# Kernel tuning notes

Measured on AMD Instinct MI355X. Metric: run time of the kernel, lower is better.

## Reference

```python
import jax, jax.numpy as jnp
import numpy as np

PAD = 1
THRESH = 10.0


def setup_inputs() -> dict:
    key = jax.random.key(0)
    k1, k2, k3 = jax.random.split(key, 3)
    x = jax.random.normal(k1, (8, 16, 62, 62), dtype=jnp.float32)
    W = jax.random.normal(k2, (32, 16, 3, 3), dtype=jnp.float32)
    b = jax.random.normal(k3, (32,), dtype=jnp.float32)
    return {"x": x, "W": W, "b": b}


def reference(x, W, b):
    # ZeroPad2d(padding) on all four sides
    x = jnp.pad(x, ((0, 0), (0, 0), (PAD, PAD), (PAD, PAD)))
    T, C, xr, xc = x.shape
    O, _, wr, wc = W.shape
    L = xr * xc

    # get_xfft_thresh: 1D FFT over flattened HxW, zero coeffs with |Re| < thresh
    xf = jnp.fft.fft(x.reshape(T, C, L))                      # (T,C,L) complex
    xf = jnp.where(jnp.abs(xf.real) < THRESH, jnp.zeros_like(xf), xf)

    # get_Wfft: zero-pad kernel to (xr,xc) bottom/right, flatten, reverse along
    # length (flipud(flip([0,1])) nets to a flip of the last axis only), then FFT
    Wp = jnp.pad(W, ((0, 0), (0, 0), (0, xr - wr), (0, xc - wc))).reshape(O, C, L)
    Wf = jnp.fft.fft(Wp[:, :, ::-1])                          # (O,C,L) complex

    # fftConv1D, batched over (image, out_channel):
    y = jnp.fft.ifft(xf[:, None, :, :] * Wf[None, :, :, :]).real  # (T,O,C,L)
    # torch.roll(y, 1) with no dims rolls the FLATTENED (C*L) tensor by 1
    y = jnp.roll(y.reshape(T, O, C * L), 1, axis=-1).reshape(T, O, C, xr, xc)
    y = y.sum(axis=2)                                         # sum over in-channels
    ans_r, ans_c = xr - wr + 1, xc - wc + 1
    y = y[:, :, :ans_r, :ans_c]
    return y + b[None, :, None, None]
```

## Files before the change

kernel.cpp:

```cpp
#include <hip/hip_runtime.h>
#include <math.h>

#define TWO_PI 6.28318530717958647692f
#define NT     1024
#define RPW    4
#define PITCH  65
#define THRESH 10.0f
#define C64    0.995184726672196886f
#define S64    0.098017140329560602f
#define C4096  0.999998823451701879f
#define S4096  0.001533980186284766f

typedef float v2f __attribute__((ext_vector_type(2)));

__device__ __forceinline__ int brev6(int x) {
    return (int)(__brev((unsigned)x) >> 26);
}

__device__ __forceinline__ v2f cmul_add(v2f a, v2f b, v2f acc) {
    acc += (v2f){a.x, a.x} * b;
    acc += (v2f){a.y, a.y} * (v2f){-b.y, b.x};
    return acc;
}

template<int R>
__device__ __forceinline__ void fft64_dif(float (&re)[R], float (&im)[R],
                                          int lane, float sign) {
    #pragma unroll
    for (int h = 32; h >= 1; h >>= 1) {
        int j = lane & (h - 1);
        float ang = sign * (TWO_PI / 64.0f) * (float)(j * (32 / h));
        float wr, wi;
        __sincosf(ang, &wi, &wr);
        bool upper = (lane & h) != 0;
        float cwr = upper ? wr : 1.0f;
        float cwi = upper ? wi : 0.0f;
        float sgn = upper ? -1.0f : 1.0f;
        #pragma unroll
        for (int m = 0; m < R; ++m) {
            float orr = __shfl_xor(re[m], h, 64);
            float oii = __shfl_xor(im[m], h, 64);
            float ar = fmaf(sgn, re[m], orr);
            float ai = fmaf(sgn, im[m], oii);
            re[m] = ar * cwr - ai * cwi;
            im[m] = ar * cwi + ai * cwr;
        }
    }
}

template<int R>
__device__ __forceinline__ void fft64_dit(float (&re)[R], float (&im)[R],
                                          int lane, float sign) {
    #pragma unroll
    for (int h = 1; h <= 32; h <<= 1) {
        int j = lane & (h - 1);
        float ang = sign * (TWO_PI / 64.0f) * (float)(j * (32 / h));
        float wr, wi;
        __sincosf(ang, &wi, &wr);
        bool upper = (lane & h) != 0;
        float cwr = upper ? wr : 1.0f;
        float cwi = upper ? wi : 0.0f;
        float sgn = upper ? -1.0f : 1.0f;
        #pragma unroll
        for (int m = 0; m < R; ++m) {
            float tr = re[m] * cwr - im[m] * cwi;
            float ti = re[m] * cwi + im[m] * cwr;
            float orr = __shfl_xor(tr, h, 64);
            float oii = __shfl_xor(ti, h, 64);
            re[m] = fmaf(sgn, tr, orr);
            im[m] = fmaf(sgn, ti, oii);
        }
    }
}

__global__ __launch_bounds__(NT) void fwdA_kernel(const float* __restrict__ x,
                                                  float2* __restrict__ Xa) {
    __shared__ float sre[64 * 33];
    __shared__ float sim[64 * 33];
    const int task = blockIdx.x >> 1;
    const int h    = blockIdx.x & 1;
    const int tid  = threadIdx.x;
    const int lane = tid & 63;
    const int w    = tid >> 6;
    const float* xr = x + (size_t)task * 62 * 62;
    for (int idx = tid; idx < 64 * 32; idx += NT) {
        int r = idx >> 5, j = idx & 31;
        int n2 = 32 * h + j;
        float v = 0.0f;
        if (r >= 1 && r <= 62 && n2 >= 1 && n2 <= 62)
            v = xr[(r - 1) * 62 + (n2 - 1)];
        sre[r * 33 + j] = v;
    }
    __syncthreads();
    float re[2], im[2];
    #pragma unroll
    for (int m = 0; m < 2; ++m) {
        re[m] = sre[lane * 33 + (w * 2 + m)];
        im[m] = 0.0f;
    }
    fft64_dif<2>(re, im, lane, -1.0f);
    __syncthreads();
    const int k1 = brev6(lane);
    #pragma unroll
    for (int m = 0; m < 2; ++m) {
        int j  = w * 2 + m;
        int n2 = 32 * h + j;
        float cr, ci;
        __sincosf(-(TWO_PI / 4096.0f) * (float)(k1 * n2), &ci, &cr);
        sre[k1 * 33 + j] = re[m] * cr - im[m] * ci;
        sim[k1 * 33 + j] = re[m] * ci + im[m] * cr;
    }
    __syncthreads();
    float2* Arow = Xa + (size_t)task * 4096;
    for (int idx = tid; idx < 64 * 32; idx += NT) {
        int k = idx >> 5, j = idx & 31;
        Arow[k * 64 + 32 * h + j] = make_float2(sre[k * 33 + j], sim[k * 33 + j]);
    }
}

__global__ __launch_bounds__(NT) void fwdB_kernel(const float2* __restrict__ Xa,
                                                  float2* __restrict__ X) {
    const int task = blockIdx.x >> 1;
    const int h    = blockIdx.x & 1;
    const int tid  = threadIdx.x;
    const int lane = tid & 63;
    const int w    = tid >> 6;
    const float2* Arow = Xa + (size_t)task * 4096;
    float re[2], im[2];
    #pragma unroll
    for (int m = 0; m < 2; ++m) {
        float2 xv = Arow[(32 * h + w * 2 + m) * 64 + lane];
        re[m] = xv.x; im[m] = xv.y;
    }
    fft64_dif<2>(re, im, lane, -1.0f);
    float2* Xrow = X + (size_t)task * 4096;
    #pragma unroll
    for (int m = 0; m < 2; ++m) {
        float rr = re[m], ii = im[m];
        if (fabsf(rr) < THRESH) { rr = 0.0f; ii = 0.0f; }
        Xrow[(32 * h + w * 2 + m) * 64 + lane] = make_float2(rr, ii);
    }
}

__global__ __launch_bounds__(NT, 4) void conv_kernel(const float2* __restrict__ X,
                                                     const float* __restrict__ W,
                                                     const float* __restrict__ b,
                                                     float* __restrict__ out) {
    __shared__ float sre[64 * PITCH];
    __shared__ float sim[64 * PITCH];
    const int t    = blockIdx.x >> 5;
    const int o    = blockIdx.x & 31;
    const int tid  = threadIdx.x;
    const int lane = tid & 63;
    const int w    = tid >> 6;

    const int k2 = brev6(lane);
    float elr, eli;
    __sincosf((TWO_PI / 64.0f) * (float)k2, &eli, &elr);

    v2f uv[RPW], vv[RPW], v2v[RPW];
    {
        float cur, cui, cvr, cvi;
        __sincosf((TWO_PI / 16.0f) * (float)w, &cui, &cur);
        __sincosf((TWO_PI / 1024.0f) * (float)w, &cvi, &cvr);
        #pragma unroll
        for (int m = 0; m < RPW; ++m) {
            uv[m] = (v2f){cur, cui};
            float vvr = cvr * elr - cvi * eli;
            float vvi = cvr * eli + cvi * elr;
            vv[m]  = (v2f){vvr, vvi};
            v2v[m] = (v2f){vvr * vvr - vvi * vvi, 2.0f * vvr * vvi};
            float nur = cur * C64 - cui * S64;
            cui = cur * S64 + cui * C64; cur = nur;
            float nvr = cvr * C4096 - cvi * S4096;
            cvi = cvr * S4096 + cvi * C4096; cvr = nvr;
        }
    }

    v2f S[RPW];
    #pragma unroll
    for (int m = 0; m < RPW; ++m) S[m] = (v2f){0.0f, 0.0f};

    const float2* Xt = X + (size_t)t * 16 * 4096 + (w * (RPW * 64) + lane);
    const float*  wo = W + o * 144;

    v2f xb[RPW];
    #pragma unroll
    for (int m = 0; m < RPW; ++m) {
        float2 q = Xt[m * 64];
        xb[m] = (v2f){q.x, q.y};
    }
    #pragma unroll 1
    for (int c = 0; c < 16; ++c) {
        v2f xn[RPW];
        if (c < 15) {
            const float2* xp = Xt + (c + 1) * 4096;
            #pragma unroll
            for (int m = 0; m < RPW; ++m) {
                float2 q = xp[m * 64];
                xn[m] = (v2f){q.x, q.y};
            }
        }
        const float wa0 = wo[c*9+0], wa1 = wo[c*9+1], wa2 = wo[c*9+2];
        const float wa3 = wo[c*9+3], wa4 = wo[c*9+4], wa5 = wo[c*9+5];
        const float wa6 = wo[c*9+6], wa7 = wo[c*9+7], wa8 = wo[c*9+8];
        #pragma unroll
        for (int m = 0; m < RPW; ++m) {
            v2f v = vv[m], v2 = v2v[m], u = uv[m];
            v2f h0 = (v2f){wa0, 0.0f}; h0 += v * wa1; h0 += v2 * wa2;
            v2f h1 = (v2f){wa3, 0.0f}; h1 += v * wa4; h1 += v2 * wa5;
            v2f h2 = (v2f){wa6, 0.0f}; h2 += v * wa7; h2 += v2 * wa8;
            v2f in = cmul_add(u, h2, h1);
            v2f P  = cmul_add(u, in, h0);
            S[m]   = cmul_add(xb[m], P, S[m]);
        }
        #pragma unroll
        for (int m = 0; m < RPW; ++m) xb[m] = xn[m];
    }

    float re[RPW], im[RPW];
    #pragma unroll
    for (int m = 0; m < RPW; ++m) { re[m] = S[m].x; im[m] = S[m].y; }
    fft64_dit<RPW>(re, im, lane, +1.0f);
    {
        float cr, ci, sr, si;
        __sincosf((TWO_PI / 1024.0f) * (float)(lane * w), &ci, &cr);
        __sincosf((TWO_PI / 4096.0f) * (float)lane, &si, &sr);
        #pragma unroll
        for (int m = 0; m < RPW; ++m) {
            float rr = re[m] * cr - im[m] * ci;
            im[m]    = re[m] * ci + im[m] * cr;
            re[m]    = rr;
            float nr = cr * sr - ci * si;
            ci = cr * si + ci * sr; cr = nr;
        }
    }
    #pragma unroll
    for (int m = 0; m < RPW; ++m) {
        int k1 = w * RPW + m;
        sre[k1 * PITCH + lane] = re[m];
        sim[k1 * PITCH + lane] = im[m];
    }
    __syncthreads();
    #pragma unroll
    for (int m = 0; m < RPW; ++m) {
        int n2 = w * RPW + m;
        re[m] = sre[lane * PITCH + n2];
        im[m] = sim[lane * PITCH + n2];
    }
    fft64_dif<RPW>(re, im, lane, +1.0f);
    __syncthreads();
    const int n1 = brev6(lane);
    #pragma unroll
    for (int m = 0; m < RPW; ++m) {
        int n2 = w * RPW + m;
        sre[n1 * PITCH + n2] = re[m];
    }
    __syncthreads();
    const float bias = b[o];
    float* orow = out + (size_t)blockIdx.x * 62 * 62;
    for (int idx = tid; idx < 62 * 62; idx += NT) {
        int r = idx / 62, s = idx - r * 62;
        orow[idx] = sre[r * PITCH + s] * (1.0f / 4096.0f) + bias;
    }
}

extern "C" void kernel_launch(void* const* d_in, const int* in_sizes, int n_in,
                              void* d_out, int out_size, void* d_ws, size_t ws_size,
                              hipStream_t stream) {
    const float* x = (const float*)d_in[0];
    const float* W = (const float*)d_in[1];
    const float* b = (const float*)d_in[2];
    float* out = (float*)d_out;
    float2* Xa = (float2*)d_ws;
    float2* X  = Xa + 128 * 4096;

    fwdA_kernel<<<dim3(256), dim3(NT), 0, stream>>>(x, Xa);
    fwdB_kernel<<<dim3(256), dim3(NT), 0, stream>>>(Xa, X);
    conv_kernel<<<dim3(256), dim3(NT), 0, stream>>>(X, W, b, out);
}
```

Before: 86.39 us.

## Exploit Hermitian symmetry to compute only half the spectrum in forward FFT and conv

The forward FFT stage now stores and processes only rows 0..32 of the 64x64 spectrum, since the input is real. The conv kernel accumulates the frequency product for only those 33 rows and rebuilds the conjugate-symmetric half from shared memory before the inverse FFT. This roughly halves the per-channel complex multiply-accumulate work and the X traffic. In exchange it adds an extra shared-memory round trip with two barriers, plus divergent work for the lone middle row handled by wave 0. The symmetry only holds if the threshold mask preserves conjugate pairs, which it does because it tests only |Re|.

After: 82.87 us. 4.1% less time.

```diff
diff --git a/kernel.cpp b/kernel.cpp
--- a/kernel.cpp
+++ b/kernel.cpp
@@ -6,10 +6,8 @@
 #define RPW    4
 #define PITCH  65
 #define THRESH 10.0f
-#define C64    0.995184726672196886f
-#define S64    0.098017140329560602f
-#define C4096  0.999998823451701879f
-#define S4096  0.001533980186284766f
+#define C128   0.998795456205172393f
+#define S128   0.049067674327418015f
 
 typedef float v2f __attribute__((ext_vector_type(2)));
 
@@ -114,7 +112,9 @@
     float2* Arow = Xa + (size_t)task * 4096;
     for (int idx = tid; idx < 64 * 32; idx += NT) {
         int k = idx >> 5, j = idx & 31;
-        Arow[k * 64 + 32 * h + j] = make_float2(sre[k * 33 + j], sim[k * 33 + j]);
+        if (k <= 32)
+            Arow[k * 64 + 32 * h + j] =
+                make_float2(sre[k * 33 + j], sim[k * 33 + j]);
     }
 }
 
@@ -125,20 +125,25 @@
     const int tid  = threadIdx.x;
     const int lane = tid & 63;
     const int w    = tid >> 6;
+    if (h == 1 && w > 0) return;
     const float2* Arow = Xa + (size_t)task * 4096;
     float re[2], im[2];
     #pragma unroll
     for (int m = 0; m < 2; ++m) {
-        float2 xv = Arow[(32 * h + w * 2 + m) * 64 + lane];
+        int row = 32 * h + w * 2 + m;
+        float2 xv = (row <= 32) ? Arow[row * 64 + lane] : make_float2(0.f, 0.f);
         re[m] = xv.x; im[m] = xv.y;
     }
     fft64_dif<2>(re, im, lane, -1.0f);
     float2* Xrow = X + (size_t)task * 4096;
     #pragma unroll
     for (int m = 0; m < 2; ++m) {
-        float rr = re[m], ii = im[m];
-        if (fabsf(rr) < THRESH) { rr = 0.0f; ii = 0.0f; }
-        Xrow[(32 * h + w * 2 + m) * 64 + lane] = make_float2(rr, ii);
+        int row = 32 * h + w * 2 + m;
+        if (row <= 32) {
+            float rr = re[m], ii = im[m];
+            if (fabsf(rr) < THRESH) { rr = 0.0f; ii = 0.0f; }
+            Xrow[row * 64 + lane] = make_float2(rr, ii);
+        }
     }
 }
 
@@ -158,69 +163,86 @@
     float elr, eli;
     __sincosf((TWO_PI / 64.0f) * (float)k2, &eli, &elr);
 
-    v2f uv[RPW], vv[RPW], v2v[RPW];
-    {
-        float cur, cui, cvr, cvi;
-        __sincosf((TWO_PI / 16.0f) * (float)w, &cui, &cur);
-        __sincosf((TWO_PI / 1024.0f) * (float)w, &cvi, &cvr);
-        #pragma unroll
-        for (int m = 0; m < RPW; ++m) {
-            uv[m] = (v2f){cur, cui};
-            float vvr = cvr * elr - cvi * eli;
-            float vvi = cvr * eli + cvi * elr;
-            vv[m]  = (v2f){vvr, vvi};
-            v2v[m] = (v2f){vvr * vvr - vvi * vvi, 2.0f * vvr * vvi};
-            float nur = cur * C64 - cui * S64;
-            cui = cur * S64 + cui * C64; cur = nur;
-            float nvr = cvr * C4096 - cvi * S4096;
-            cvi = cvr * S4096 + cvi * C4096; cvr = nvr;
-        }
-    }
-
-    v2f S[RPW];
-    #pragma unroll
-    for (int m = 0; m < RPW; ++m) S[m] = (v2f){0.0f, 0.0f};
-
-    const float2* Xt = X + (size_t)t * 16 * 4096 + (w * (RPW * 64) + lane);
+    const int rA = 2 * w, rB = 2 * w + 1;
+    float uAr, uAi, vAr, vAi, uBr, uBi, vBr, vBi;
+    __sincosf((TWO_PI / 64.0f) * (float)rA, &uAi, &uAr);
+    __sincosf((TWO_PI / 4096.0f) * (float)rA, &vAi, &vAr);
+    __sincosf((TWO_PI / 64.0f) * (float)rB, &uBi, &uBr);
+    __sincosf((TWO_PI / 4096.0f) * (float)rB, &vBi, &vBr);
+    v2f uA = {uAr, uAi};
+    v2f vA = {vAr * elr - vAi * eli, vAr * eli + vAi * elr};
+    v2f v2A = {vA.x * vA.x - vA.y * vA.y, 2.0f * vA.x * vA.y};
+    v2f uB = {uBr, uBi};
+    v2f vB = {vBr * elr - vBi * eli, vBr * eli + vBi * elr};
+    v2f v2B = {vB.x * vB.x - vB.y * vB.y, 2.0f * vB.x * vB.y};
+    v2f vC = {C128 * elr - S128 * eli, C128 * eli + S128 * elr};
+    v2f v2C = {vC.x * vC.x - vC.y * vC.y, 2.0f * vC.x * vC.y};
+
+    v2f SA = {0,0}, SB = {0,0}, SC = {0,0};
+
+    const float2* Xt = X + (size_t)t * 16 * 4096 + lane;
     const float*  wo = W + o * 144;
 
-    v2f xb[RPW];
-    #pragma unroll
-    for (int m = 0; m < RPW; ++m) {
-        float2 q = Xt[m * 64];
-        xb[m] = (v2f){q.x, q.y};
-    }
+    v2f xbA, xbB, xbC;
+    { float2 q = Xt[rA * 64]; xbA = (v2f){q.x, q.y}; }
+    { float2 q = Xt[rB * 64]; xbB = (v2f){q.x, q.y}; }
+    if (w == 0) { float2 q = Xt[32 * 64]; xbC = (v2f){q.x, q.y}; }
     #pragma unroll 1
     for (int c = 0; c < 16; ++c) {
-        v2f xn[RPW];
+        v2f xnA, xnB, xnC;
         if (c < 15) {
-            const float2* xp = Xt + (c + 1) * 4096;
-            #pragma unroll
-            for (int m = 0; m < RPW; ++m) {
-                float2 q = xp[m * 64];
-                xn[m] = (v2f){q.x, q.y};
-            }
+            { float2 q = Xt[(c + 1) * 4096 + rA * 64]; xnA = (v2f){q.x, q.y}; }
+            { float2 q = Xt[(c + 1) * 4096 + rB * 64]; xnB = (v2f){q.x, q.y}; }
+            if (w == 0) { float2 q = Xt[(c + 1) * 4096 + 32 * 64]; xnC = (v2f){q.x, q.y}; }
         }
         const float wa0 = wo[c*9+0], wa1 = wo[c*9+1], wa2 = wo[c*9+2];
         const float wa3 = wo[c*9+3], wa4 = wo[c*9+4], wa5 = wo[c*9+5];
         const float wa6 = wo[c*9+6], wa7 = wo[c*9+7], wa8 = wo[c*9+8];
-        #pragma unroll
-        for (int m = 0; m < RPW; ++m) {
-            v2f v = vv[m], v2 = v2v[m], u = uv[m];
-            v2f h0 = (v2f){wa0, 0.0f}; h0 += v * wa1; h0 += v2 * wa2;
-            v2f h1 = (v2f){wa3, 0.0f}; h1 += v * wa4; h1 += v2 * wa5;
-            v2f h2 = (v2f){wa6, 0.0f}; h2 += v * wa7; h2 += v2 * wa8;
-            v2f in = cmul_add(u, h2, h1);
-            v2f P  = cmul_add(u, in, h0);
-            S[m]   = cmul_add(xb[m], P, S[m]);
-        }
-        #pragma unroll
-        for (int m = 0; m < RPW; ++m) xb[m] = xn[m];
-    }
+        {
+            v2f h0 = (v2f){wa0, 0.0f}; h0 += vA * wa1; h0 += v2A * wa2;
+            v2f h1 = (v2f){wa3, 0.0f}; h1 += vA * wa4; h1 += v2A * wa5;
+            v2f h2 = (v2f){wa6, 0.0f}; h2 += vA * wa7; h2 += v2A * wa8;
+            v2f P  = cmul_add(uA, cmul_add(uA, h2, h1), h0);
+            SA = cmul_add(xbA, P, SA);
+        }
+        {
+            v2f h0 = (v2f){wa0, 0.0f}; h0 += vB * wa1; h0 += v2B * wa2;
+            v2f h1 = (v2f){wa3, 0.0f}; h1 += vB * wa4; h1 += v2B * wa5;
+            v2f h2 = (v2f){wa6, 0.0f}; h2 += vB * wa7; h2 += v2B * wa8;
+            v2f P  = cmul_add(uB, cmul_add(uB, h2, h1), h0);
+            SB = cmul_add(xbB, P, SB);
+        }
+        if (w == 0) {
+            v2f h0 = (v2f){wa0, 0.0f}; h0 += vC * wa1; h0 += v2C * wa2;
+            v2f h1 = (v2f){wa3, 0.0f}; h1 += vC * wa4; h1 += v2C * wa5;
+            v2f h2 = (v2f){wa6, 0.0f}; h2 += vC * wa7; h2 += v2C * wa8;
+            v2f P  = h0 - h1 + h2;
+            SC = cmul_add(xbC, P, SC);
+        }
+        xbA = xnA; xbB = xnB;
+        if (w == 0) xbC = xnC;
+    }
+
+    sre[rA * PITCH + k2] = SA.x; sim[rA * PITCH + k2] = SA.y;
+    sre[rB * PITCH + k2] = SB.x; sim[rB * PITCH + k2] = SB.y;
+    if (w == 0) { sre[32 * PITCH + k2] = SC.x; sim[32 * PITCH + k2] = SC.y; }
+    __syncthreads();
 
     float re[RPW], im[RPW];
     #pragma unroll
-    for (int m = 0; m < RPW; ++m) { re[m] = S[m].x; im[m] = S[m].y; }
+    for (int m = 0; m < RPW; ++m) {
+        int k1 = w * RPW + m;
+        if (k1 <= 32) {
+            re[m] = sre[k1 * PITCH + k2];
+            im[m] = sim[k1 * PITCH + k2];
+        } else {
+            int k1p = 64 - k1, k2p = 63 - k2;
+            re[m] =  sre[k1p * PITCH + k2p];
+            im[m] = -sim[k1p * PITCH + k2p];
+        }
+    }
+    __syncthreads();
+
     fft64_dit<RPW>(re, im, lane, +1.0f);
     {
         float cr, ci, sr, si;
```
